# Kernel optimization log

Hardware: AMD Instinct MI355X
Metric: run time of the kernel (lower is better)

## Reference

```python
import jax, jax.numpy as jnp
import numpy as np

B, T, I, H = 256, 2048, 128, 64  # batch, seq_len, input_size, hidden_size
NL = 3  # num LSTM layers


def setup_inputs() -> dict:
    key = jax.random.key(0)
    ks = jax.random.split(key, 2 + 4 * NL + 2)
    s = 1.0 / np.sqrt(H)  # PyTorch LSTM/Linear init scale
    d = {"x": jax.random.normal(ks[0], (B, T, I), jnp.float32)}
    in_dims = [I, H, H]
    for l in range(NL):
        k0, k1, k2, k3 = ks[1 + 4 * l : 5 + 4 * l]
        d[f"w_ih{l}"] = jax.random.uniform(k0, (4 * H, in_dims[l]), jnp.float32, -s, s)
        d[f"w_hh{l}"] = jax.random.uniform(k1, (4 * H, H), jnp.float32, -s, s)
        d[f"b_ih{l}"] = jax.random.uniform(k2, (4 * H,), jnp.float32, -s, s)
        d[f"b_hh{l}"] = jax.random.uniform(k3, (4 * H,), jnp.float32, -s, s)
    d["fc_w"] = jax.random.uniform(ks[-2], (1, H), jnp.float32, -s, s)
    d["fc_b"] = jax.random.uniform(ks[-1], (1,), jnp.float32, -s, s)
    return d


def _lstm_layer(x, w_ih, w_hh, b_ih, b_hh):
    # Precompute input contribution for all timesteps: [B, T, 4H]
    pre = jnp.einsum('bti,gi->btg', x, w_ih) + b_ih + b_hh

    def step(carry, p_t):  # p_t: [B, 4H]
        h, c = carry
        gates = p_t + h @ w_hh.T
        i, f, g, o = jnp.split(gates, 4, axis=-1)  # PyTorch gate order i,f,g,o
        i = jax.nn.sigmoid(i)
        f = jax.nn.sigmoid(f)
        g = jnp.tanh(g)
        o = jax.nn.sigmoid(o)
        c = f * c + i * g
        h = o * jnp.tanh(c)
        return (h, c), h

    h0 = jnp.zeros((x.shape[0], H), x.dtype)
    _, hs = jax.lax.scan(step, (h0, h0), jnp.swapaxes(pre, 0, 1))  # hs: [T, B, H]
    return jnp.swapaxes(hs, 0, 1)  # [B, T, H]


def reference(x, w_ih0, w_hh0, b_ih0, b_hh0,
              w_ih1, w_hh1, b_ih1, b_hh1,
              w_ih2, w_hh2, b_ih2, b_hh2,
              fc_w, fc_b):
    h = _lstm_layer(x, w_ih0, w_hh0, b_ih0, b_hh0)
    h = _lstm_layer(h, w_ih1, w_hh1, b_ih1, b_hh1)
    h = _lstm_layer(h, w_ih2, w_hh2, b_ih2, b_hh2)
    h = h.reshape(-1, H)  # [B*T, H]
    return h @ fc_w.T + fc_b  # [B*T, 1]
```

## Files before the change

kernel.cpp:

```cpp
#include <hip/hip_runtime.h>

#define TT 2048
#define BB 256
#define HID 64

__device__ __forceinline__ float frcp(float x) { return __builtin_amdgcn_rcpf(x); }
__device__ __forceinline__ float fsig(float x) { return frcp(1.f + __expf(-x)); }
__device__ __forceinline__ float ftanh(float x) { return 1.f - 2.f * frcp(1.f + __expf(2.f * x)); }

__global__ __launch_bounds__(256, 2) void gemm_pre_k(
    const float* __restrict__ in, const float* __restrict__ W,
    const float* __restrict__ b_ih, const float* __restrict__ b_hh,
    float* __restrict__ out, int K)
{
    __shared__ __align__(16) float in_s[64][20];
    __shared__ __align__(16) float w_s[16][256];

    const int tid = threadIdx.x;
    const int tx = tid & 15, ty = tid >> 4;
    const long long row0 = (long long)blockIdx.x * 64;

    float4 bias[4];
    {
        const float4* bi4 = (const float4*)b_ih;
        const float4* bh4 = (const float4*)b_hh;
#pragma unroll
        for (int jj = 0; jj < 4; ++jj) {
            float4 a = bi4[tx * 4 + jj], b = bh4[tx * 4 + jj];
            bias[jj] = make_float4(a.x + b.x, a.y + b.y, a.z + b.z, a.w + b.w);
        }
    }

    float4 acc[4][4];
#pragma unroll
    for (int i = 0; i < 4; ++i)
#pragma unroll
        for (int j = 0; j < 4; ++j) acc[i][j] = make_float4(0.f, 0.f, 0.f, 0.f);

    const int rs = tid >> 2;
    const int kq = tid & 3;

    for (int kc = 0; kc < K; kc += 16) {
        __syncthreads();
        float4 iv = *(const float4*)(in + (row0 + rs) * K + kc + kq * 4);
        *(float4*)(&in_s[rs][kq * 4]) = iv;
        const float* wr = W + (long long)tid * K + kc;
        float4 w0 = ((const float4*)wr)[0];
        float4 w1 = ((const float4*)wr)[1];
        float4 w2 = ((const float4*)wr)[2];
        float4 w3 = ((const float4*)wr)[3];
        w_s[0][tid] = w0.x;  w_s[1][tid] = w0.y;  w_s[2][tid] = w0.z;  w_s[3][tid] = w0.w;
        w_s[4][tid] = w1.x;  w_s[5][tid] = w1.y;  w_s[6][tid] = w1.z;  w_s[7][tid] = w1.w;
        w_s[8][tid] = w2.x;  w_s[9][tid] = w2.y;  w_s[10][tid] = w2.z; w_s[11][tid] = w2.w;
        w_s[12][tid] = w3.x; w_s[13][tid] = w3.y; w_s[14][tid] = w3.z; w_s[15][tid] = w3.w;
        __syncthreads();

#pragma unroll
        for (int k2 = 0; k2 < 4; ++k2) {
            float4 a[4];
#pragma unroll
            for (int i = 0; i < 4; ++i) a[i] = *(const float4*)(&in_s[ty * 4 + i][k2 * 4]);
#pragma unroll
            for (int kk = 0; kk < 4; ++kk) {
                const int k = k2 * 4 + kk;
                float4 wv[4];
#pragma unroll
                for (int jj = 0; jj < 4; ++jj) wv[jj] = *(const float4*)(&w_s[k][tx * 16 + jj * 4]);
#pragma unroll
                for (int i = 0; i < 4; ++i) {
                    const float av = ((const float*)&a[i])[kk];
#pragma unroll
                    for (int jj = 0; jj < 4; ++jj) {
                        acc[i][jj].x += av * wv[jj].x;
                        acc[i][jj].y += av * wv[jj].y;
                        acc[i][jj].z += av * wv[jj].z;
                        acc[i][jj].w += av * wv[jj].w;
                    }
                }
            }
        }
    }

#pragma unroll
    for (int i = 0; i < 4; ++i) {
        float4* op = (float4*)(out + (row0 + ty * 4 + i) * 256 + tx * 16);
#pragma unroll
        for (int jj = 0; jj < 4; ++jj) {
            float4 v = acc[i][jj];
            v.x += bias[jj].x; v.y += bias[jj].y; v.z += bias[jj].z; v.w += bias[jj].w;
            op[jj] = v;
        }
    }
}

__global__ __launch_bounds__(256) void lstm_rec_k(
    const float* __restrict__ pre, const float* __restrict__ w_hh,
    float* __restrict__ h_out, float* __restrict__ out,
    const float* __restrict__ fc_w, const float* __restrict__ fc_b,
    int mode)
{
    __shared__ __align__(16) float h_s[HID];
    __shared__ float gate_s[256];

    const int g = threadIdx.x;
    const int b = blockIdx.x;

    float4 w4[16];
    const float4* wr = (const float4*)(w_hh + g * HID);
#pragma unroll
    for (int k = 0; k < 16; ++k) w4[k] = wr[k];

    float fcw = 0.f, fcb = 0.f;
    if (mode == 2 && g < HID) { fcw = fc_w[g]; fcb = fc_b[0]; }
    if (g < HID) h_s[g] = 0.f;
    float c = 0.f;

    const float* pp = pre + (long long)b * TT * 256 + g;
    float p_next = pp[0];
    float* hop = (mode == 2) ? nullptr : (h_out + (long long)b * TT * HID + g);
    float* oop = (mode == 2) ? (out + (long long)b * TT) : nullptr;
    __syncthreads();

    for (int t = 0; t < TT; ++t) {
        float acc = p_next;
        if (t + 1 < TT) p_next = pp[256];
        pp += 256;

        const float4* h4 = (const float4*)h_s;
        float s0 = 0.f, s1 = 0.f, s2 = 0.f, s3 = 0.f;
#pragma unroll
        for (int k = 0; k < 16; ++k) {
            float4 hv = h4[k];
            s0 += w4[k].x * hv.x;
            s1 += w4[k].y * hv.y;
            s2 += w4[k].z * hv.z;
            s3 += w4[k].w * hv.w;
        }
        acc += (s0 + s1) + (s2 + s3);

        float a = (g >= 128 && g < 192) ? ftanh(acc) : fsig(acc);
        gate_s[g] = a;
        __syncthreads();

        if (g < HID) {
            float iv = gate_s[g], fv = gate_s[g + 64], gv = gate_s[g + 128], ov = gate_s[g + 192];
            c = fv * c + iv * gv;
            float h = ov * ftanh(c);
            h_s[g] = h;
            if (mode == 2) {
                float v = h * fcw;
#pragma unroll
                for (int off = 32; off > 0; off >>= 1) v += __shfl_down(v, off);
                if (g == 0) oop[t] = v + fcb;
            } else {
                hop[(long long)t * HID] = h;
            }
        }
        __syncthreads();
    }
}

extern "C" void kernel_launch(void* const* d_in, const int* in_sizes, int n_in,
                              void* d_out, int out_size, void* d_ws, size_t ws_size,
                              hipStream_t stream)
{
    const float* x    = (const float*)d_in[0];
    const float* wih0 = (const float*)d_in[1];
    const float* whh0 = (const float*)d_in[2];
    const float* bih0 = (const float*)d_in[3];
    const float* bhh0 = (const float*)d_in[4];
    const float* wih1 = (const float*)d_in[5];
    const float* whh1 = (const float*)d_in[6];
    const float* bih1 = (const float*)d_in[7];
    const float* bhh1 = (const float*)d_in[8];
    const float* wih2 = (const float*)d_in[9];
    const float* whh2 = (const float*)d_in[10];
    const float* bih2 = (const float*)d_in[11];
    const float* bhh2 = (const float*)d_in[12];
    const float* fcw  = (const float*)d_in[13];
    const float* fcb  = (const float*)d_in[14];
    float* outp = (float*)d_out;

    const long long R = (long long)BB * TT;
    float* pre  = (float*)d_ws;
    float* hbuf = pre + R * 256;

    const int gemm_grid = (int)(R / 64);

    gemm_pre_k<<<gemm_grid, 256, 0, stream>>>(x, wih0, bih0, bhh0, pre, 128);
    lstm_rec_k<<<BB, 256, 0, stream>>>(pre, whh0, hbuf, nullptr, nullptr, nullptr, 0);
    gemm_pre_k<<<gemm_grid, 256, 0, stream>>>(hbuf, wih1, bih1, bhh1, pre, 64);
    lstm_rec_k<<<BB, 256, 0, stream>>>(pre, whh1, hbuf, nullptr, nullptr, nullptr, 1);
    gemm_pre_k<<<gemm_grid, 256, 0, stream>>>(hbuf, wih2, bih2, bhh2, pre, 64);
    lstm_rec_k<<<BB, 256, 0, stream>>>(pre, whh2, nullptr, outp, fcw, fcb, 2);
}
```

Baseline: 5.297 ms.

## Batch 16 sequences per block and compute LSTM recurrence with split-fp16 MFMA

Replaces the one-sequence-per-block scalar recurrence with a kernel where each block handles 16 batch rows and computes h@W_hh^T via 16x16x32 f16 MFMA. fp32 accuracy is approximated by splitting both weights and hidden state into hi/lo fp16 parts and doing three MFMAs per tile. The hidden state goes through a double-buffered, XOR-swizzled LDS array, which cuts the step to one barrier, and the next step's pre-activation is prefetched into registers. The grid shrinks from 256 blocks to 16, so far fewer CUs are busy, and the hi/lo split carries a small precision risk.

```diff
diff --git a/kernel.cpp b/kernel.cpp
--- a/kernel.cpp
+++ b/kernel.cpp
@@ -3,6 +3,10 @@
 #define TT 2048
 #define BB 256
 #define HID 64
+#define NB 16
+
+typedef _Float16 half8 __attribute__((ext_vector_type(8)));
+typedef float f32x4 __attribute__((ext_vector_type(4)));
 
 __device__ __forceinline__ float frcp(float x) { return __builtin_amdgcn_rcpf(x); }
 __device__ __forceinline__ float fsig(float x) { return frcp(1.f + __expf(-x)); }
@@ -93,70 +97,139 @@
     }
 }
 
-__global__ __launch_bounds__(256) void lstm_rec_k(
+__global__ __launch_bounds__(256) void lstm_rec_mfma(
     const float* __restrict__ pre, const float* __restrict__ w_hh,
     float* __restrict__ h_out, float* __restrict__ out,
     const float* __restrict__ fc_w, const float* __restrict__ fc_b,
     int mode)
 {
-    __shared__ __align__(16) float h_s[HID];
-    __shared__ float gate_s[256];
-
-    const int g = threadIdx.x;
-    const int b = blockIdx.x;
-
-    float4 w4[16];
-    const float4* wr = (const float4*)(w_hh + g * HID);
-#pragma unroll
-    for (int k = 0; k < 16; ++k) w4[k] = wr[k];
-
-    float fcw = 0.f, fcb = 0.f;
-    if (mode == 2 && g < HID) { fcw = fc_w[g]; fcb = fc_b[0]; }
-    if (g < HID) h_s[g] = 0.f;
-    float c = 0.f;
-
-    const float* pp = pre + (long long)b * TT * 256 + g;
-    float p_next = pp[0];
-    float* hop = (mode == 2) ? nullptr : (h_out + (long long)b * TT * HID + g);
-    float* oop = (mode == 2) ? (out + (long long)b * TT) : nullptr;
+    __shared__ half8 HEX[2][16][16];
+    __shared__ float FCP[2][4][16];
+
+    const int tid = threadIdx.x;
+    const int w = tid >> 6, lane = tid & 63;
+    const int n = lane & 15, quad = lane >> 4;
+    const int blk = blockIdx.x;
+    const long long b = (long long)blk * NB + n;
+
+    HEX[0][tid >> 4][tid & 15] = (half8){0, 0, 0, 0, 0, 0, 0, 0};
+
+    half8 Ahi[4][2], Alo[4][2];
+#pragma unroll
+    for (int m = 0; m < 4; ++m) {
+        const int row = 16 * (w + 4 * m) + n;
+#pragma unroll
+        for (int kt = 0; kt < 2; ++kt) {
+            const float* wp_ = w_hh + row * 64 + 32 * kt + 8 * quad;
+            f32x4 a0 = *(const f32x4*)wp_;
+            f32x4 a1 = *(const f32x4*)(wp_ + 4);
+            half8 hi, lo;
+#pragma unroll
+            for (int j = 0; j < 4; ++j) {
+                _Float16 h0 = (_Float16)a0[j];
+                _Float16 h1 = (_Float16)a1[j];
+                hi[j] = h0;     lo[j] = (_Float16)(a0[j] - (float)h0);
+                hi[4 + j] = h1; lo[4 + j] = (_Float16)(a1[j] - (float)h1);
+            }
+            Ahi[m][kt] = hi; Alo[m][kt] = lo;
+        }
+    }
+
+    f32x4 fw = {0.f, 0.f, 0.f, 0.f};
+    float fcbv = 0.f;
+    if (mode == 2) {
+        fw = *(const f32x4*)(fc_w + 16 * w + 4 * quad);
+        fcbv = fc_b[0];
+    }
+
+    const float* pt = pre + (b * TT) * 256 + 16 * w + 4 * quad;
+    f32x4 pre_c[4];
+#pragma unroll
+    for (int m = 0; m < 4; ++m) pre_c[m] = *(const f32x4*)(pt + m * 64);
+
+    float* hob = (mode != 2) ? (h_out + (b * TT) * 64 + 16 * w + 4 * quad) : nullptr;
+    float* oob = (mode == 2) ? (out + (long long)(blk * NB) * TT) : nullptr;
+
+    float cst[4] = {0.f, 0.f, 0.f, 0.f};
+
     __syncthreads();
 
     for (int t = 0; t < TT; ++t) {
-        float acc = p_next;
-        if (t + 1 < TT) p_next = pp[256];
-        pp += 256;
-
-        const float4* h4 = (const float4*)h_s;
-        float s0 = 0.f, s1 = 0.f, s2 = 0.f, s3 = 0.f;
-#pragma unroll
-        for (int k = 0; k < 16; ++k) {
-            float4 hv = h4[k];
-            s0 += w4[k].x * hv.x;
-            s1 += w4[k].y * hv.y;
-            s2 += w4[k].z * hv.z;
-            s3 += w4[k].w * hv.w;
-        }
-        acc += (s0 + s1) + (s2 + s3);
-
-        float a = (g >= 128 && g < 192) ? ftanh(acc) : fsig(acc);
-        gate_s[g] = a;
+        const int p = t & 1;
+
+        half8 Bhi[2], Blo[2];
+#pragma unroll
+        for (int kt = 0; kt < 2; ++kt) {
+            const int s0 = (2 * kt + (quad >> 1)) * 4 + 2 * (quad & 1);
+            const int col = n ^ (s0 >> 1);
+            half8 c0 = HEX[p][s0][col];
+            half8 c1 = HEX[p][s0 + 1][col];
+            Bhi[kt] = __builtin_shufflevector(c0, c1, 0, 1, 2, 3, 8, 9, 10, 11);
+            Blo[kt] = __builtin_shufflevector(c0, c1, 4, 5, 6, 7, 12, 13, 14, 15);
+        }
+
+        const float* pn = pt + ((t + 1 < TT) ? 256 : 0);
+        f32x4 pre_n[4];
+#pragma unroll
+        for (int m = 0; m < 4; ++m) pre_n[m] = *(const f32x4*)(pn + m * 64);
+
+        f32x4 G[4];
+#pragma unroll
+        for (int m = 0; m < 4; ++m) {
+            f32x4 C = pre_c[m];
+#pragma unroll
+            for (int kt = 0; kt < 2; ++kt) {
+                C = __builtin_amdgcn_mfma_f32_16x16x32_f16(Ahi[m][kt], Bhi[kt], C, 0, 0, 0);
+                C = __builtin_amdgcn_mfma_f32_16x16x32_f16(Ahi[m][kt], Blo[kt], C, 0, 0, 0);
+                C = __builtin_amdgcn_mfma_f32_16x16x32_f16(Alo[m][kt], Bhi[kt], C, 0, 0, 0);
+            }
+            G[m] = C;
+        }
+
+        float hv[4];
+#pragma unroll
+        for (int r = 0; r < 4; ++r) {
+            float iv = fsig(G[0][r]);
+            float fv = fsig(G[1][r]);
+            float gv = ftanh(G[2][r]);
+            float ov = fsig(G[3][r]);
+            cst[r] = fv * cst[r] + iv * gv;
+            hv[r] = ov * ftanh(cst[r]);
+        }
+
+        {
+            half8 pk;
+#pragma unroll
+            for (int r = 0; r < 4; ++r) {
+                _Float16 hh = (_Float16)hv[r];
+                pk[r] = hh;
+                pk[4 + r] = (_Float16)(hv[r] - (float)hh);
+            }
+            const int s = w * 4 + quad;
+            HEX[p ^ 1][s][n ^ (s >> 1)] = pk;
+        }
+
+        if (mode != 2) {
+            f32x4 ho = {hv[0], hv[1], hv[2], hv[3]};
+            *(f32x4*)hob = ho;
+            hob += 64;
+        } else {
+            float s = fw[0] * hv[0] + fw[1] * hv[1] + fw[2] * hv[2] + fw[3] * hv[3];
+            s += __shfl_down(s, 32);
+            s += __shfl_down(s, 16);
+            if (quad == 0) FCP[p][w][n] = s;
+        }
+
         __syncthreads();
 
-        if (g < HID) {
-            float iv = gate_s[g], fv = gate_s[g + 64], gv = gate_s[g + 128], ov = gate_s[g + 192];
-            c = fv * c + iv * gv;
-            float h = ov * ftanh(c);
-            h_s[g] = h;
-            if (mode == 2) {
-                float v = h * fcw;
-#pragma unroll
-                for (int off = 32; off > 0; off >>= 1) v += __shfl_down(v, off);
-                if (g == 0) oop[t] = v + fcb;
-            } else {
-                hop[(long long)t * HID] = h;
-            }
-        }
-        __syncthreads();
+        if (mode == 2 && w == 0 && lane < 16) {
+            oob[(long long)lane * TT + t] =
+                fcbv + FCP[p][0][lane] + FCP[p][1][lane] + FCP[p][2][lane] + FCP[p][3][lane];
+        }
+
+#pragma unroll
+        for (int m = 0; m < 4; ++m) pre_c[m] = pre_n[m];
+        pt = pn;
     }
 }
 
@@ -186,11 +259,12 @@
     float* hbuf = pre + R * 256;
 
     const int gemm_grid = (int)(R / 64);
+    const int rec_grid = BB / NB;
 
     gemm_pre_k<<<gemm_grid, 256, 0, stream>>>(x, wih0, bih0, bhh0, pre, 128);
-    lstm_rec_k<<<BB, 256, 0, stream>>>(pre, whh0, hbuf, nullptr, nullptr, nullptr, 0);
+    lstm_rec_mfma<<<rec_grid, 256, 0, stream>>>(pre, whh0, hbuf, nullptr, nullptr, nullptr, 0);
     gemm_pre_k<<<gemm_grid, 256, 0, stream>>>(hbuf, wih1, bih1, bhh1, pre, 64);
-    lstm_rec_k<<<BB, 256, 0, stream>>>(pre, whh1, hbuf, nullptr, nullptr, nullptr, 1);
+    lstm_rec_mfma<<<rec_grid, 256, 0, stream>>>(pre, whh1, hbuf, nullptr, nullptr, nullptr, 1);
     gemm_pre_k<<<gemm_grid, 256, 0, stream>>>(hbuf, wih2, bih2, bhh2, pre, 64);
-    lstm_rec_k<<<BB, 256, 0, stream>>>(pre, whh2, nullptr, outp, fcw, fcb, 2);
+    lstm_rec_mfma<<<rec_grid, 256, 0, stream>>>(pre, whh2, nullptr, outp, fcw, fcb, 2);
 }
```

New measurement: 7.926 ms. 1.5x slower.
